# Optimization experiments

Hardware: AMD Instinct MI355X
Metric: run time of the kernel (lower is better)

## Reference

```python
import jax, jax.numpy as jnp
import numpy as np
from jax import lax

K = 3
STRIDE = 2
PADDING = 1
OUTPUT_PADDING = 1


def setup_inputs() -> dict:
    key = jax.random.key(0)
    k1, k2, k3, k4 = jax.random.split(key, 4)
    B, C, H, W = 4, 64, 128, 128
    outC = 64
    g_ch = 3
    x = jax.random.normal(k1, (B, C, H, W), dtype=jnp.float32)
    guide = jax.random.normal(k2, (B, g_ch, H * STRIDE, W * STRIDE), dtype=jnp.float32)
    # kaiming-uniform-like init scale: bound = 1/sqrt(fan_in), fan_in = C*K*K
    fan_in = C * K * K
    bound = 1.0 / np.sqrt(fan_in)
    weight = jax.random.uniform(k3, (C, outC, K, K), dtype=jnp.float32, minval=-bound, maxval=bound)
    bias = jax.random.uniform(k4, (outC,), dtype=jnp.float32, minval=-bound, maxval=bound)
    return {"x": x, "guide": guide, "weight": weight, "bias": bias}


def _patches(t, pad):
    # torch.nn.functional.unfold equivalent: channel ordering (C, kh, kw)
    return lax.conv_general_dilated_patches(
        t, filter_shape=(K, K), window_strides=(1, 1), padding=[(pad, pad), (pad, pad)]
    )


def reference(x, guide, weight, bias):
    B, C, H, W = x.shape
    _, g_ch, GH, GW = guide.shape
    s, p, op = STRIDE, PADDING, OUTPUT_PADDING

    # Gaussian affinity kernel from guide patches
    gp = (K - 1) // 2
    guide_unf = _patches(guide, gp).reshape(B, g_ch, K * K, GH, GW)
    diff = guide_unf - guide_unf[:, :, K * K // 2 : K * K // 2 + 1]
    kern = jnp.exp(-0.5 * jnp.sum(diff * diff, axis=1))  # [B, K*K, GH, GW]
    kern = kern.reshape(B, 1, K, K, GH, GW)

    # depthwise transposed conv with all-ones 1x1 kernel == zero-stuffing upsample
    Ht, Wt = (H - 1) * s + 1, (W - 1) * s + 1
    temp = jnp.zeros((B, C, Ht, Wt), dtype=x.dtype).at[:, :, ::s, ::s].set(x)
    pad = (K - 1) - p
    temp = jnp.pad(temp, ((0, 0), (0, 0), (pad, pad + op), (pad, pad + op)))

    cols = _patches(temp, 0).reshape(B, C, K, K, GH, GW)
    in_mul_k = cols * kern  # [B, C, K, K, GH, GW]
    out = jnp.einsum("bcklhw,cokl->bohw", in_mul_k, weight)
    return out + bias.reshape(1, -1, 1, 1)
```

## Files before the change

kernel.cpp:

```cpp
#include <hip/hip_runtime.h>
#include <math.h>

typedef __attribute__((ext_vector_type(8))) short short8;
typedef __attribute__((ext_vector_type(4))) float float4v;

#define GH_ 256
#define GW_ 256
#define H_  128
#define W_  128
#define C_  64
#define OC_ 64
#define NB_ 4

static __device__ __forceinline__ unsigned short f2bf(float f) {
    union { float f; unsigned int u; } v; v.f = f;
    unsigned int u = v.u;
    unsigned int r = u + 0x7FFFu + ((u >> 16) & 1u);
    return (unsigned short)(r >> 16);
}

__global__ __launch_bounds__(256) void prep(const float* __restrict__ x,
                                            const float* __restrict__ w,
                                            unsigned short* __restrict__ xbf,
                                            unsigned short* __restrict__ wtb) {
    int b = blockIdx.z;
    int tid = threadIdx.x;
    if (b == 4) {
        int flat = (blockIdx.y * 2 + blockIdx.x) * 256 + tid;
        if (flat < 9 * OC_ * C_) {
            int c = flat & 63, o = (flat >> 6) & 63, t = flat >> 12;
            int kh = t / 3, kw = t - kh * 3;
            wtb[flat] = f2bf(w[((c * OC_ + o) * 3 + kh) * 3 + kw]);
        }
        return;
    }
    int half = blockIdx.x, ih = blockIdx.y;
    __shared__ float xl[C_][65];
    int iw0 = half * 64;
    for (int i = tid; i < C_ * 64; i += 256) {
        int c = i >> 6, iw = i & 63;
        xl[c][iw] = x[(((b * C_ + c) * H_) + ih) * W_ + iw0 + iw];
    }
    __syncthreads();
    for (int i = tid; i < 64 * 32; i += 256) {
        int iw = i >> 5, cp = i & 31;
        unsigned int lo = f2bf(xl[2 * cp][iw]);
        unsigned int hi = f2bf(xl[2 * cp + 1][iw]);
        unsigned int* dst = (unsigned int*)(xbf +
            ((size_t)((b * H_ + ih) * W_ + iw0 + iw)) * C_);
        dst[cp] = lo | (hi << 16);
    }
}

__global__ __launch_bounds__(256) void pac_kern(const float* __restrict__ guide,
                                                float* __restrict__ ktab) {
    const int yp  = blockIdx.x;
    const int cls = blockIdx.y;
    const int b   = blockIdx.z;
    const int hp = cls >> 1, wp = cls & 1;
    const int ntap = (1 + hp) * (1 + wp);
    const int tid = threadIdx.x;
    const int h = 2 * yp + hp;
    const float* gb = guide + (size_t)b * 3 * GH_ * GW_;

    for (int i = tid; i < ntap * 128; i += 256) {
        int xp = i & 127, tap = i >> 7;
        int r, q;
        if (wp == 0) { r = tap; q = 0; }
        else         { r = tap >> 1; q = tap & 1; }
        int w = 2 * xp + wp;
        int rr = yp + r, cl = xp + q;
        float kv = 0.f;
        if (rr < H_ && cl < W_) {
            int hh = rr * 2, ww = cl * 2;
            float s2 = 0.f;
            #pragma unroll
            for (int g = 0; g < 3; ++g) {
                float d = gb[(g * GH_ + hh) * GW_ + ww] - gb[(g * GH_ + h) * GW_ + w];
                s2 += d * d;
            }
            kv = __expf(-0.5f * s2);
        }
        ktab[(((size_t)((b * 4 + cls) * 4 + tap)) << 14) + (yp << 7) + xp] = kv;
    }
}

__global__ __launch_bounds__(512, 2) void pac_main(
    const unsigned short* __restrict__ xbf,
    const float* __restrict__ ktab,
    const unsigned short* __restrict__ wtb,
    const float* __restrict__ bias,
    float* __restrict__ out)
{
    const int ypair = blockIdx.x;
    const int hp    = blockIdx.y;
    const int b     = blockIdx.z;
    const int tid = threadIdx.x;

    const int wave = tid >> 6, lane = tid & 63;
    const int l16 = lane & 15, qk = lane >> 4;
    const int oh  = wave & 1;
    const int py  = (wave >> 1) & 1;
    const int xh  = wave >> 2;
    const int obase = oh * 32;
    const int xpb   = xh * 64;
    const int yp = ypair * 2 + py;
    const int h  = 2 * yp + hp;

    const float* kt0 = ktab + ((size_t)((b * 4 + hp * 2 + 0) * 4) << 14) + (yp << 7);
    const float* kt1 = ktab + ((size_t)((b * 4 + hp * 2 + 1) * 4) << 14) + (yp << 7);

    float acc0[2][4][4];
    float acc1[2][4][4];
    #pragma unroll
    for (int mf = 0; mf < 2; ++mf)
        #pragma unroll
        for (int nf = 0; nf < 4; ++nf)
            #pragma unroll
            for (int e = 0; e < 4; ++e) { acc0[mf][nf][e] = 0.f; acc1[mf][nf][e] = 0.f; }

    for (int r = 0; r <= hp; ++r) {
        int kh = hp ? 2 * r : 1;
        int row = yp + r; if (row > H_ - 1) row = H_ - 1;

        short8 af[3][2][2];
        #pragma unroll
        for (int kw3 = 0; kw3 < 3; ++kw3) {
            const short8* wbase = (const short8*)(wtb + (size_t)(kh * 3 + kw3) * OC_ * C_);
            #pragma unroll
            for (int mf = 0; mf < 2; ++mf) {
                int o = obase + mf * 16 + l16;
                af[kw3][mf][0] = wbase[(o * C_ + qk * 8) >> 3];
                af[kw3][mf][1] = wbase[(o * C_ + 32 + qk * 8) >> 3];
            }
        }

        #pragma unroll
        for (int nf = 0; nf < 4; ++nf) {
            int xp = xpb + nf * 16 + l16;
            int col0 = xp;
            int col1 = xp + 1; if (col1 > W_ - 1) col1 = W_ - 1;
            const short8* xb0 = (const short8*)(xbf +
                ((size_t)((b * H_ + row) * W_ + col0)) * C_);
            const short8* xb1 = (const short8*)(xbf +
                ((size_t)((b * H_ + row) * W_ + col1)) * C_);
            short8 b0a = xb0[qk],     b0b = xb0[4 + qk];
            short8 b1a = xb1[qk],     b1b = xb1[4 + qk];
            float kc = kt0[(r << 14) + xp];
            float kl = kt1[((2 * r) << 14) + xp];
            float kr = kt1[((2 * r + 1) << 14) + xp];
            #pragma unroll
            for (int mf = 0; mf < 2; ++mf) {
                float4v d;
                d = (float4v){0.f, 0.f, 0.f, 0.f};
                d = __builtin_amdgcn_mfma_f32_16x16x32_bf16(af[1][mf][0], b0a, d, 0, 0, 0);
                d = __builtin_amdgcn_mfma_f32_16x16x32_bf16(af[1][mf][1], b0b, d, 0, 0, 0);
                #pragma unroll
                for (int e = 0; e < 4; ++e) acc0[mf][nf][e] += kc * d[e];
                d = (float4v){0.f, 0.f, 0.f, 0.f};
                d = __builtin_amdgcn_mfma_f32_16x16x32_bf16(af[0][mf][0], b0a, d, 0, 0, 0);
                d = __builtin_amdgcn_mfma_f32_16x16x32_bf16(af[0][mf][1], b0b, d, 0, 0, 0);
                #pragma unroll
                for (int e = 0; e < 4; ++e) acc1[mf][nf][e] += kl * d[e];
                d = (float4v){0.f, 0.f, 0.f, 0.f};
                d = __builtin_amdgcn_mfma_f32_16x16x32_bf16(af[2][mf][0], b1a, d, 0, 0, 0);
                d = __builtin_amdgcn_mfma_f32_16x16x32_bf16(af[2][mf][1], b1b, d, 0, 0, 0);
                #pragma unroll
                for (int e = 0; e < 4; ++e) acc1[mf][nf][e] += kr * d[e];
            }
        }
    }

    float bv[2][4];
    #pragma unroll
    for (int mf = 0; mf < 2; ++mf)
        #pragma unroll
        for (int e = 0; e < 4; ++e)
            bv[mf][e] = bias[obase + mf * 16 + qk * 4 + e];

    #pragma unroll
    for (int mf = 0; mf < 2; ++mf)
        #pragma unroll
        for (int e = 0; e < 4; ++e) {
            int o = obase + mf * 16 + qk * 4 + e;
            float2* op = (float2*)(out + (((size_t)b * OC_ + o) * GH_ + h) * GW_);
            #pragma unroll
            for (int nf = 0; nf < 4; ++nf) {
                int xp = xpb + nf * 16 + l16;
                float2 v;
                v.x = acc0[mf][nf][e] + bv[mf][e];
                v.y = acc1[mf][nf][e] + bv[mf][e];
                op[xp] = v;
            }
        }
}

extern "C" void kernel_launch(void* const* d_in, const int* in_sizes, int n_in,
                              void* d_out, int out_size, void* d_ws, size_t ws_size,
                              hipStream_t stream) {
    const float* x     = (const float*)d_in[0];
    const float* guide = (const float*)d_in[1];
    const float* wgt   = (const float*)d_in[2];
    const float* bias  = (const float*)d_in[3];
    float* out = (float*)d_out;

    unsigned short* xbf = (unsigned short*)d_ws;
    unsigned short* wtb = xbf + (size_t)NB_ * H_ * W_ * C_;
    size_t koff = (size_t)NB_ * H_ * W_ * C_ + 9 * OC_ * C_;
    float* ktab = (float*)(xbf + koff);

    prep<<<dim3(2, 128, 5), 256, 0, stream>>>(x, wgt, xbf, wtb);
    pac_kern<<<dim3(128, 4, 4), 256, 0, stream>>>(guide, ktab);
    pac_main<<<dim3(64, 2, 4), 512, 0, stream>>>(xbf, ktab, wtb, bias, out);
}
```

Before: 125.7 us.

## Split pac_main into smaller blocks and process kw taps sequentially to cut registers

Each block now covers a single output row with 256 threads instead of two rows with 512, which doubles the grid. The three kw taps are handled one at a time, so only one set of weight fragments and one set of x fragments is live at once, not all three. This is meant to lower register pressure and raise occupancy. In exchange, the x row is reloaded for the center and left taps and the MFMA work is split into separate loops, which may lose some instruction-level overlap.

```diff
diff --git a/kernel.cpp b/kernel.cpp
--- a/kernel.cpp
+++ b/kernel.cpp
@@ -85,26 +85,24 @@
     }
 }
 
-__global__ __launch_bounds__(512, 2) void pac_main(
+__global__ __launch_bounds__(256) void pac_main(
     const unsigned short* __restrict__ xbf,
     const float* __restrict__ ktab,
     const unsigned short* __restrict__ wtb,
     const float* __restrict__ bias,
     float* __restrict__ out)
 {
-    const int ypair = blockIdx.x;
-    const int hp    = blockIdx.y;
-    const int b     = blockIdx.z;
+    const int yp = blockIdx.x;
+    const int hp = blockIdx.y;
+    const int b  = blockIdx.z;
     const int tid = threadIdx.x;
 
     const int wave = tid >> 6, lane = tid & 63;
     const int l16 = lane & 15, qk = lane >> 4;
     const int oh  = wave & 1;
-    const int py  = (wave >> 1) & 1;
-    const int xh  = wave >> 2;
+    const int xh  = wave >> 1;
     const int obase = oh * 32;
     const int xpb   = xh * 64;
-    const int yp = ypair * 2 + py;
     const int h  = 2 * yp + hp;
 
     const float* kt0 = ktab + ((size_t)((b * 4 + hp * 2 + 0) * 4) << 14) + (yp << 7);
@@ -122,51 +120,82 @@
     for (int r = 0; r <= hp; ++r) {
         int kh = hp ? 2 * r : 1;
         int row = yp + r; if (row > H_ - 1) row = H_ - 1;
-
-        short8 af[3][2][2];
-        #pragma unroll
-        for (int kw3 = 0; kw3 < 3; ++kw3) {
-            const short8* wbase = (const short8*)(wtb + (size_t)(kh * 3 + kw3) * OC_ * C_);
+        const short8* xrow = (const short8*)(xbf + ((size_t)((b * H_ + row) * W_)) * C_);
+
+        {
+            const short8* wbase = (const short8*)(wtb + (size_t)(kh * 3 + 1) * OC_ * C_);
+            short8 af[2][2];
             #pragma unroll
             for (int mf = 0; mf < 2; ++mf) {
                 int o = obase + mf * 16 + l16;
-                af[kw3][mf][0] = wbase[(o * C_ + qk * 8) >> 3];
-                af[kw3][mf][1] = wbase[(o * C_ + 32 + qk * 8) >> 3];
-            }
-        }
-
-        #pragma unroll
-        for (int nf = 0; nf < 4; ++nf) {
-            int xp = xpb + nf * 16 + l16;
-            int col0 = xp;
-            int col1 = xp + 1; if (col1 > W_ - 1) col1 = W_ - 1;
-            const short8* xb0 = (const short8*)(xbf +
-                ((size_t)((b * H_ + row) * W_ + col0)) * C_);
-            const short8* xb1 = (const short8*)(xbf +
-                ((size_t)((b * H_ + row) * W_ + col1)) * C_);
-            short8 b0a = xb0[qk],     b0b = xb0[4 + qk];
-            short8 b1a = xb1[qk],     b1b = xb1[4 + qk];
-            float kc = kt0[(r << 14) + xp];
-            float kl = kt1[((2 * r) << 14) + xp];
-            float kr = kt1[((2 * r + 1) << 14) + xp];
+                af[mf][0] = wbase[(o * C_ + qk * 8) >> 3];
+                af[mf][1] = wbase[(o * C_ + 32 + qk * 8) >> 3];
+            }
+            #pragma unroll
+            for (int nf = 0; nf < 4; ++nf) {
+                int xp = xpb + nf * 16 + l16;
+                const short8* xb = xrow + xp * 8;
+                short8 ba = xb[qk], bb = xb[4 + qk];
+                float kv = kt0[(r << 14) + xp];
+                #pragma unroll
+                for (int mf = 0; mf < 2; ++mf) {
+                    float4v d = {0.f, 0.f, 0.f, 0.f};
+                    d = __builtin_amdgcn_mfma_f32_16x16x32_bf16(af[mf][0], ba, d, 0, 0, 0);
+                    d = __builtin_amdgcn_mfma_f32_16x16x32_bf16(af[mf][1], bb, d, 0, 0, 0);
+                    #pragma unroll
+                    for (int e = 0; e < 4; ++e) acc0[mf][nf][e] += kv * d[e];
+                }
+            }
+        }
+        {
+            const short8* wbase = (const short8*)(wtb + (size_t)(kh * 3 + 0) * OC_ * C_);
+            short8 af[2][2];
             #pragma unroll
             for (int mf = 0; mf < 2; ++mf) {
-                float4v d;
-                d = (float4v){0.f, 0.f, 0.f, 0.f};
-                d = __builtin_amdgcn_mfma_f32_16x16x32_bf16(af[1][mf][0], b0a, d, 0, 0, 0);
-                d = __builtin_amdgcn_mfma_f32_16x16x32_bf16(af[1][mf][1], b0b, d, 0, 0, 0);
+                int o = obase + mf * 16 + l16;
+                af[mf][0] = wbase[(o * C_ + qk * 8) >> 3];
+                af[mf][1] = wbase[(o * C_ + 32 + qk * 8) >> 3];
+            }
+            #pragma unroll
+            for (int nf = 0; nf < 4; ++nf) {
+                int xp = xpb + nf * 16 + l16;
+                const short8* xb = xrow + xp * 8;
+                short8 ba = xb[qk], bb = xb[4 + qk];
+                float kv = kt1[((2 * r) << 14) + xp];
                 #pragma unroll
-                for (int e = 0; e < 4; ++e) acc0[mf][nf][e] += kc * d[e];
-                d = (float4v){0.f, 0.f, 0.f, 0.f};
-                d = __builtin_amdgcn_mfma_f32_16x16x32_bf16(af[0][mf][0], b0a, d, 0, 0, 0);
-                d = __builtin_amdgcn_mfma_f32_16x16x32_bf16(af[0][mf][1], b0b, d, 0, 0, 0);
+                for (int mf = 0; mf < 2; ++mf) {
+                    float4v d = {0.f, 0.f, 0.f, 0.f};
+                    d = __builtin_amdgcn_mfma_f32_16x16x32_bf16(af[mf][0], ba, d, 0, 0, 0);
+                    d = __builtin_amdgcn_mfma_f32_16x16x32_bf16(af[mf][1], bb, d, 0, 0, 0);
+                    #pragma unroll
+                    for (int e = 0; e < 4; ++e) acc1[mf][nf][e] += kv * d[e];
+                }
+            }
+        }
+        {
+            const short8* wbase = (const short8*)(wtb + (size_t)(kh * 3 + 2) * OC_ * C_);
+            short8 af[2][2];
+            #pragma unroll
+            for (int mf = 0; mf < 2; ++mf) {
+                int o = obase + mf * 16 + l16;
+                af[mf][0] = wbase[(o * C_ + qk * 8) >> 3];
+                af[mf][1] = wbase[(o * C_ + 32 + qk * 8) >> 3];
+            }
+            #pragma unroll
+            for (int nf = 0; nf < 4; ++nf) {
+                int xp = xpb + nf * 16 + l16;
+                int col = xp + 1; if (col > W_ - 1) col = W_ - 1;
+                const short8* xb = xrow + col * 8;
+                short8 ba = xb[qk], bb = xb[4 + qk];
+                float kv = kt1[((2 * r + 1) << 14) + xp];
                 #pragma unroll
-                for (int e = 0; e < 4; ++e) acc1[mf][nf][e] += kl * d[e];
-                d = (float4v){0.f, 0.f, 0.f, 0.f};
-                d = __builtin_amdgcn_mfma_f32_16x16x32_bf16(af[2][mf][0], b1a, d, 0, 0, 0);
-                d = __builtin_amdgcn_mfma_f32_16x16x32_bf16(af[2][mf][1], b1b, d, 0, 0, 0);
-                #pragma unroll
-                for (int e = 0; e < 4; ++e) acc1[mf][nf][e] += kr * d[e];
+                for (int mf = 0; mf < 2; ++mf) {
+                    float4v d = {0.f, 0.f, 0.f, 0.f};
+                    d = __builtin_amdgcn_mfma_f32_16x16x32_bf16(af[mf][0], ba, d, 0, 0, 0);
+                    d = __builtin_amdgcn_mfma_f32_16x16x32_bf16(af[mf][1], bb, d, 0, 0, 0);
+                    #pragma unroll
+                    for (int e = 0; e < 4; ++e) acc1[mf][nf][e] += kv * d[e];
+                }
             }
         }
     }
@@ -211,5 +240,5 @@
 
     prep<<<dim3(2, 128, 5), 256, 0, stream>>>(x, wgt, xbf, wtb);
     pac_kern<<<dim3(128, 4, 4), 256, 0, stream>>>(guide, ktab);
-    pac_main<<<dim3(64, 2, 4), 512, 0, stream>>>(xbf, ktab, wtb, bias, out);
-}
+    pac_main<<<dim3(128, 2, 4), 256, 0, stream>>>(xbf, ktab, wtb, bias, out);
+}
```

Result: faster. 121.9 us (-3.0%).
